# Performance work log

Measured on AMD Instinct MI355X. Metric: run time of the kernel, lower is better.

## Reference

```python
import jax, jax.numpy as jnp
import numpy as np

N, D_IN, D_OUT = 4096, 1024, 1024


def setup_inputs() -> dict:
    key = jax.random.key(0)
    kx, kq, kk, kv = jax.random.split(key, 4)
    s = 1.0 / np.sqrt(D_IN)
    return {
        "x": jax.random.normal(kx, (N, D_IN), dtype=jnp.float32),
        "Wq": jax.random.normal(kq, (D_OUT, D_IN), dtype=jnp.float32) * s,
        "Wk": jax.random.normal(kk, (D_OUT, D_IN), dtype=jnp.float32) * s,
        "Wv": jax.random.normal(kv, (D_OUT, D_IN), dtype=jnp.float32) * s,
    }


def reference(x, Wq, Wk, Wv):
    # nn.Linear(d_in, d_out, bias=False): y = x @ W.T with W: [d_out, d_in]
    q = x @ Wq.T            # [N, d_out]
    k = x @ Wk.T            # [N, d_out]
    v = x @ Wv.T            # [N, d_out]
    scores = q @ k.T        # [N, N]
    scale = 1.0 / jnp.sqrt(jnp.asarray(k.shape[-1], dtype=x.dtype))
    attn = jax.nn.softmax(scores * scale, axis=-1)
    return attn @ v         # [N, d_out]
```

## Files before the change

kernel.cpp:

```cpp
#include <hip/hip_runtime.h>


typedef __attribute__((ext_vector_type(8))) __bf16 bf16x8;
typedef __attribute__((ext_vector_type(4))) float floatx4;

#define GLB_AS __attribute__((address_space(1)))
#define LDS_AS __attribute__((address_space(3)))

static __device__ __forceinline__ unsigned short f2bf_u16(float f) {
  union { float f; unsigned u; } x; x.f = f;
  unsigned r = x.u;
  r += 0x7fffu + ((r >> 16) & 1u);
  return (unsigned short)(r >> 16);
}
static __device__ __forceinline__ float bf2f(unsigned short u) {
  union { unsigned u; float f; } x; x.u = ((unsigned)u) << 16; return x.f;
}

__global__ __launch_bounds__(256) void cast_all(const float* __restrict__ x,
                                                const float* __restrict__ Wq,
                                                const float* __restrict__ Wk,
                                                const float* __restrict__ Wv,
                                                unsigned short* __restrict__ xb,
                                                unsigned short* __restrict__ wb) {
  const int i = blockIdx.x * 256 + threadIdx.x;
  const int NX4 = 4096 * 1024 / 4;
  const int NW4 = 1024 * 1024 / 4;
  const float* src; unsigned short* dst; int k;
  if (i < NX4)                { src = x;  dst = xb;                   k = i; }
  else if (i < NX4 + NW4)     { src = Wq; dst = wb;                   k = i - NX4; }
  else if (i < NX4 + 2 * NW4) { src = Wk; dst = wb + 1024 * 1024;     k = i - NX4 - NW4; }
  else                        { src = Wv; dst = wb + 2 * 1024 * 1024; k = i - NX4 - 2 * NW4; }
  float4 v = reinterpret_cast<const float4*>(src)[k];
  ushort4 o = make_ushort4(f2bf_u16(v.x), f2bf_u16(v.y), f2bf_u16(v.z), f2bf_u16(v.w));
  reinterpret_cast<ushort4*>(dst)[k] = o;
}

struct GemmOuts { void* c[4]; int ldc[4]; };

template <int EPI>
__global__ __launch_bounds__(256, 2) void gemm_bt(const unsigned short* __restrict__ A,
                                                  const unsigned short* __restrict__ B,
                                                  GemmOuts outs, int lda, int ldb,
                                                  int klen, float scale) {
  __shared__ unsigned short sh[24576];
  const int t = threadIdx.x;
  const int w = t >> 6, lane = t & 63;
  const int wm = w >> 1, wn = w & 1;
  const int gx = gridDim.x;
  const int nwg = gx * gridDim.y;
  int bid = blockIdx.y * gx + blockIdx.x;
  bid = (bid & 7) * (nwg >> 3) + (bid >> 3);
  const int row0 = (bid / gx) * 256;
  const int col0 = (bid % gx) * 128;
  const int z = blockIdx.z;
  const int kstart = z * klen;
  const int NT = klen >> 5;

  const int srow = t >> 2;
  const int scbe = (((t & 3) ^ ((t >> 3) & 3)) << 3);
  const unsigned short* gA0 = A + (size_t)(row0 + srow) * lda + kstart + scbe;
  const unsigned short* gA1 = gA0 + (size_t)64 * lda;
  const unsigned short* gA2 = gA0 + (size_t)128 * lda;
  const unsigned short* gA3 = gA0 + (size_t)192 * lda;
  const unsigned short* gB0 = B + (size_t)(col0 + srow) * ldb + kstart + scbe;
  const unsigned short* gB1 = gB0 + (size_t)64 * ldb;

#define STAGE(tl_) do { \
    const int bb_ = ((tl_) & 1) * 12288; \
    __builtin_amdgcn_global_load_lds((const GLB_AS void*)(gA0 + (tl_) * 32), \
        (LDS_AS void*)&sh[bb_ + t * 8], 16, 0, 0); \
    __builtin_amdgcn_global_load_lds((const GLB_AS void*)(gA1 + (tl_) * 32), \
        (LDS_AS void*)&sh[bb_ + 2048 + t * 8], 16, 0, 0); \
    __builtin_amdgcn_global_load_lds((const GLB_AS void*)(gA2 + (tl_) * 32), \
        (LDS_AS void*)&sh[bb_ + 4096 + t * 8], 16, 0, 0); \
    __builtin_amdgcn_global_load_lds((const GLB_AS void*)(gA3 + (tl_) * 32), \
        (LDS_AS void*)&sh[bb_ + 6144 + t * 8], 16, 0, 0); \
    __builtin_amdgcn_global_load_lds((const GLB_AS void*)(gB0 + (tl_) * 32), \
        (LDS_AS void*)&sh[bb_ + 8192 + t * 8], 16, 0, 0); \
    __builtin_amdgcn_global_load_lds((const GLB_AS void*)(gB1 + (tl_) * 32), \
        (LDS_AS void*)&sh[bb_ + 10240 + t * 8], 16, 0, 0); \
  } while (0)

  const int fr = lane & 15;
  const int sg = (((lane >> 4) ^ ((lane >> 1) & 3)) << 3);
  int aofs[8], bofs[4];
#pragma unroll
  for (int mf = 0; mf < 8; ++mf) aofs[mf] = ((wm * 128 + mf * 16 + fr) << 5) + sg;
#pragma unroll
  for (int nf = 0; nf < 4; ++nf) bofs[nf] = 8192 + ((wn * 64 + nf * 16 + fr) << 5) + sg;

  floatx4 acc[8][4] = {};

  STAGE(0);

  for (int tile = 0; tile < NT; ++tile) {
    if (tile + 1 < NT) {
      STAGE(tile + 1);
      asm volatile("s_waitcnt vmcnt(6)" ::: "memory");
    } else {
      asm volatile("s_waitcnt vmcnt(0)" ::: "memory");
    }
    __builtin_amdgcn_s_barrier();

    const int bo = (tile & 1) * 12288;
    bf16x8 af[8], bf[4];
#pragma unroll
    for (int mf = 0; mf < 8; ++mf) af[mf] = *(const bf16x8*)&sh[bo + aofs[mf]];
#pragma unroll
    for (int nf = 0; nf < 4; ++nf) bf[nf] = *(const bf16x8*)&sh[bo + bofs[nf]];
#pragma unroll
    for (int mf = 0; mf < 8; ++mf)
#pragma unroll
      for (int nf = 0; nf < 4; ++nf)
        acc[mf][nf] = __builtin_amdgcn_mfma_f32_16x16x32_bf16(af[mf], bf[nf], acc[mf][nf], 0, 0, 0);

    __builtin_amdgcn_s_barrier();
  }
#undef STAGE

  const int er = (lane >> 4) * 4;
  const int ec = lane & 15;

  if (EPI == 0) {
    unsigned short* Cb = (unsigned short*)outs.c[z];
    const int ldc = outs.ldc[z];
#pragma unroll
    for (int mf = 0; mf < 8; ++mf)
#pragma unroll
      for (int nf = 0; nf < 4; ++nf)
#pragma unroll
        for (int r = 0; r < 4; ++r)
          Cb[(size_t)(row0 + wm * 128 + mf * 16 + er + r) * ldc +
             (col0 + wn * 64 + nf * 16 + ec)] = f2bf_u16(acc[mf][nf][r] * scale);
  } else if (EPI == 2) {
    unsigned short* Pb = (unsigned short*)outs.c[0];
    float* rsp = (float*)outs.c[1];
    const int ldc = outs.ldc[0];
    const int rj = ((col0 >> 7) * 2 + wn) * 4096;
#pragma unroll
    for (int mf = 0; mf < 8; ++mf) {
#pragma unroll
      for (int r = 0; r < 4; ++r) {
        const int m = row0 + wm * 128 + mf * 16 + er + r;
        float rsum = 0.f;
#pragma unroll
        for (int nf = 0; nf < 4; ++nf) {
          const float e = __expf(acc[mf][nf][r] * scale);
          Pb[(size_t)m * ldc + (col0 + wn * 64 + nf * 16 + ec)] = f2bf_u16(e);
          rsum += e;
        }
        rsum += __shfl_xor(rsum, 1);
        rsum += __shfl_xor(rsum, 2);
        rsum += __shfl_xor(rsum, 4);
        rsum += __shfl_xor(rsum, 8);
        if (ec == 0) rsp[rj + m] = rsum;
      }
    }
  } else {
    if (col0 < 2048) {
      unsigned short* qkb = (unsigned short*)outs.c[0];
#pragma unroll
      for (int mf = 0; mf < 8; ++mf)
#pragma unroll
        for (int nf = 0; nf < 4; ++nf)
#pragma unroll
          for (int r = 0; r < 4; ++r)
            qkb[(size_t)(row0 + wm * 128 + mf * 16 + er + r) * 2048 +
                (col0 + wn * 64 + nf * 16 + ec)] = f2bf_u16(acc[mf][nf][r] * scale);
    } else {
      unsigned short* vT = (unsigned short*)outs.c[1];
#pragma unroll
      for (int mf = 0; mf < 8; ++mf)
#pragma unroll
        for (int nf = 0; nf < 4; ++nf) {
          const int n = (col0 - 2048) + wn * 64 + nf * 16 + ec;
          const int mb = row0 + wm * 128 + mf * 16 + er;
          ushort4 o = make_ushort4(f2bf_u16(acc[mf][nf][0] * scale),
                                   f2bf_u16(acc[mf][nf][1] * scale),
                                   f2bf_u16(acc[mf][nf][2] * scale),
                                   f2bf_u16(acc[mf][nf][3] * scale));
          *reinterpret_cast<ushort4*>(&vT[(size_t)n * 4096 + mb]) = o;
        }
    }
  }
}

__global__ __launch_bounds__(256) void reduce_pv(float* __restrict__ out,
                                                 const unsigned short* __restrict__ p0,
                                                 const unsigned short* __restrict__ p1,
                                                 const float* __restrict__ rsp) {
  const int row = blockIdx.x;
  const int lane = threadIdx.x & 63;
  float s = rsp[lane * 4096 + row];
#pragma unroll
  for (int off = 32; off >= 1; off >>= 1) s += __shfl_xor(s, off);
  const float inv = 1.0f / s;
  const int idx = row * 256 + threadIdx.x;
  ushort4 a = ((const ushort4*)p0)[idx];
  ushort4 b = ((const ushort4*)p1)[idx];
  float4 o;
  o.x = (bf2f(a.x) + bf2f(b.x)) * inv;
  o.y = (bf2f(a.y) + bf2f(b.y)) * inv;
  o.z = (bf2f(a.z) + bf2f(b.z)) * inv;
  o.w = (bf2f(a.w) + bf2f(b.w)) * inv;
  ((float4*)out)[idx] = o;
}

extern "C" void kernel_launch(void* const* d_in, const int* in_sizes, int n_in,
                              void* d_out, int out_size, void* d_ws, size_t ws_size,
                              hipStream_t stream) {
  const float* x  = (const float*)d_in[0];
  const float* Wq = (const float*)d_in[1];
  const float* Wk = (const float*)d_in[2];
  const float* Wv = (const float*)d_in[3];
  float* out = (float*)d_out;

  const int N = 4096, D = 1024;

  char* ws = (char*)d_ws;
  unsigned short* P   = (unsigned short*)ws;
  unsigned short* qkb = (unsigned short*)(ws + (32u << 20));
  unsigned short* vT  = (unsigned short*)(ws + (48u << 20));
  unsigned short* xb  = (unsigned short*)(ws + (56u << 20));
  unsigned short* wb  = (unsigned short*)(ws + (64u << 20));
  float*          rsp = (float*)(ws + (70u << 20));
  unsigned short* p0  = xb;
  unsigned short* p1  = (unsigned short*)(ws + (72u << 20));

  cast_all<<<7168, 256, 0, stream>>>(x, Wq, Wk, Wv, xb, wb);

  GemmOuts oq; oq.c[0] = qkb; oq.c[1] = vT; oq.c[2] = oq.c[3] = qkb;
  oq.ldc[0] = 2048; oq.ldc[1] = 4096; oq.ldc[2] = oq.ldc[3] = 2048;
  gemm_bt<3><<<dim3(3 * D / 128, N / 256, 1), 256, 0, stream>>>(xb, wb, oq, D, D, D, 1.0f);

  GemmOuts os; os.c[0] = P; os.c[1] = rsp; os.c[2] = os.c[3] = P;
  os.ldc[0] = N; os.ldc[1] = 0; os.ldc[2] = os.ldc[3] = N;
  gemm_bt<2><<<dim3(N / 128, N / 256, 1), 256, 0, stream>>>(qkb, qkb + D, os, 2 * D, 2 * D, D, 0.03125f);

  GemmOuts op;
  op.c[0] = p0; op.ldc[0] = D;
  op.c[1] = p1; op.ldc[1] = D;
  op.c[2] = p0; op.ldc[2] = D;
  op.c[3] = p1; op.ldc[3] = D;
  gemm_bt<0><<<dim3(D / 128, N / 256, 2), 256, 0, stream>>>(P, vT, op, N, N, N / 2, 1.0f);

  reduce_pv<<<N, 256, 0, stream>>>(out, p0, p1, rsp);
}
```

Baseline: 142.8 us.

## Fuse split-K reduction and normalization into PV GEMM via atomic tile counters

Replaces the separate reduce_pv pass with a last-arriving-block scheme. Each split-K block of the PV GEMM writes its bf16 partial, bumps a per-tile atomic counter, and the second block to finish sums both partials and applies the softmax row normalization straight into the fp32 output. Row sums are pre-collapsed by a small kernel, and the counters are zeroed by an extra block in the cast kernel. This removes a full read/write pass and a launch, at the cost of fences, atomics, a tail imbalance on the finishing blocks, and a new small kernel.

```diff
diff --git a/kernel.cpp b/kernel.cpp
--- a/kernel.cpp
+++ b/kernel.cpp
@@ -22,10 +22,15 @@
                                                 const float* __restrict__ Wk,
                                                 const float* __restrict__ Wv,
                                                 unsigned short* __restrict__ xb,
-                                                unsigned short* __restrict__ wb) {
-  const int i = blockIdx.x * 256 + threadIdx.x;
+                                                unsigned short* __restrict__ wb,
+                                                int* __restrict__ cnt) {
   const int NX4 = 4096 * 1024 / 4;
   const int NW4 = 1024 * 1024 / 4;
+  if (blockIdx.x == 7168) {
+    if (threadIdx.x < 128) cnt[threadIdx.x] = 0;
+    return;
+  }
+  const int i = blockIdx.x * 256 + threadIdx.x;
   const float* src; unsigned short* dst; int k;
   if (i < NX4)                { src = x;  dst = xb;                   k = i; }
   else if (i < NX4 + NW4)     { src = Wq; dst = wb;                   k = i - NX4; }
@@ -36,7 +41,16 @@
   reinterpret_cast<ushort4*>(dst)[k] = o;
 }
 
-struct GemmOuts { void* c[4]; int ldc[4]; };
+__global__ __launch_bounds__(256) void collapse_rs(const float* __restrict__ rsp,
+                                                   float* __restrict__ rs) {
+  const int r = blockIdx.x * 256 + threadIdx.x;
+  float s = 0.f;
+#pragma unroll
+  for (int j = 0; j < 64; ++j) s += rsp[j * 4096 + r];
+  rs[r] = s;
+}
+
+struct GemmOuts { void* c[5]; int ldc0; };
 
 template <int EPI>
 __global__ __launch_bounds__(256, 2) void gemm_bt(const unsigned short* __restrict__ A,
@@ -44,6 +58,7 @@
                                                   GemmOuts outs, int lda, int ldb,
                                                   int klen, float scale) {
   __shared__ unsigned short sh[24576];
+  __shared__ int lf;
   const int t = threadIdx.x;
   const int w = t >> 6, lane = t & 63;
   const int wm = w >> 1, wn = w & 1;
@@ -123,20 +138,45 @@
   const int ec = lane & 15;
 
   if (EPI == 0) {
-    unsigned short* Cb = (unsigned short*)outs.c[z];
-    const int ldc = outs.ldc[z];
+    float* Of = (float*)outs.c[0];
+    unsigned short* myp = (unsigned short*)(z == 0 ? outs.c[1] : outs.c[2]);
+    const unsigned short* otp = (const unsigned short*)(z == 0 ? outs.c[2] : outs.c[1]);
+    const float* rsv = (const float*)outs.c[3];
+    int* cnt = (int*)outs.c[4];
+    const int tileid = (row0 >> 8) * gx + (col0 >> 7);
 #pragma unroll
     for (int mf = 0; mf < 8; ++mf)
 #pragma unroll
       for (int nf = 0; nf < 4; ++nf)
 #pragma unroll
         for (int r = 0; r < 4; ++r)
-          Cb[(size_t)(row0 + wm * 128 + mf * 16 + er + r) * ldc +
-             (col0 + wn * 64 + nf * 16 + ec)] = f2bf_u16(acc[mf][nf][r] * scale);
+          myp[(size_t)(row0 + wm * 128 + mf * 16 + er + r) * 1024 +
+              (col0 + wn * 64 + nf * 16 + ec)] = f2bf_u16(acc[mf][nf][r]);
+    __threadfence();
+    __syncthreads();
+    if (t == 0) lf = atomicAdd(cnt + tileid, 1);
+    __syncthreads();
+    if (lf == 1) {
+      __threadfence();
+#pragma unroll
+      for (int mf = 0; mf < 8; ++mf) {
+#pragma unroll
+        for (int r = 0; r < 4; ++r) {
+          const int m = row0 + wm * 128 + mf * 16 + er + r;
+          const float inv = 1.0f / rsv[m];
+#pragma unroll
+          for (int nf = 0; nf < 4; ++nf) {
+            const int n = col0 + wn * 64 + nf * 16 + ec;
+            const float own = bf2f(f2bf_u16(acc[mf][nf][r]));
+            Of[(size_t)m * 1024 + n] = (own + bf2f(otp[(size_t)m * 1024 + n])) * inv;
+          }
+        }
+      }
+    }
   } else if (EPI == 2) {
     unsigned short* Pb = (unsigned short*)outs.c[0];
     float* rsp = (float*)outs.c[1];
-    const int ldc = outs.ldc[0];
+    const int ldc = outs.ldc0;
     const int rj = ((col0 >> 7) * 2 + wn) * 4096;
 #pragma unroll
     for (int mf = 0; mf < 8; ++mf) {
@@ -167,7 +207,7 @@
 #pragma unroll
           for (int r = 0; r < 4; ++r)
             qkb[(size_t)(row0 + wm * 128 + mf * 16 + er + r) * 2048 +
-                (col0 + wn * 64 + nf * 16 + ec)] = f2bf_u16(acc[mf][nf][r] * scale);
+                (col0 + wn * 64 + nf * 16 + ec)] = f2bf_u16(acc[mf][nf][r]);
     } else {
       unsigned short* vT = (unsigned short*)outs.c[1];
 #pragma unroll
@@ -176,35 +216,12 @@
         for (int nf = 0; nf < 4; ++nf) {
           const int n = (col0 - 2048) + wn * 64 + nf * 16 + ec;
           const int mb = row0 + wm * 128 + mf * 16 + er;
-          ushort4 o = make_ushort4(f2bf_u16(acc[mf][nf][0] * scale),
-                                   f2bf_u16(acc[mf][nf][1] * scale),
-                                   f2bf_u16(acc[mf][nf][2] * scale),
-                                   f2bf_u16(acc[mf][nf][3] * scale));
+          ushort4 o = make_ushort4(f2bf_u16(acc[mf][nf][0]), f2bf_u16(acc[mf][nf][1]),
+                                   f2bf_u16(acc[mf][nf][2]), f2bf_u16(acc[mf][nf][3]));
           *reinterpret_cast<ushort4*>(&vT[(size_t)n * 4096 + mb]) = o;
         }
     }
   }
-}
-
-__global__ __launch_bounds__(256) void reduce_pv(float* __restrict__ out,
-                                                 const unsigned short* __restrict__ p0,
-                                                 const unsigned short* __restrict__ p1,
-                                                 const float* __restrict__ rsp) {
-  const int row = blockIdx.x;
-  const int lane = threadIdx.x & 63;
-  float s = rsp[lane * 4096 + row];
-#pragma unroll
-  for (int off = 32; off >= 1; off >>= 1) s += __shfl_xor(s, off);
-  const float inv = 1.0f / s;
-  const int idx = row * 256 + threadIdx.x;
-  ushort4 a = ((const ushort4*)p0)[idx];
-  ushort4 b = ((const ushort4*)p1)[idx];
-  float4 o;
-  o.x = (bf2f(a.x) + bf2f(b.x)) * inv;
-  o.y = (bf2f(a.y) + bf2f(b.y)) * inv;
-  o.z = (bf2f(a.z) + bf2f(b.z)) * inv;
-  o.w = (bf2f(a.w) + bf2f(b.w)) * inv;
-  ((float4*)out)[idx] = o;
 }
 
 extern "C" void kernel_launch(void* const* d_in, const int* in_sizes, int n_in,
@@ -225,25 +242,22 @@
   unsigned short* xb  = (unsigned short*)(ws + (56u << 20));
   unsigned short* wb  = (unsigned short*)(ws + (64u << 20));
   float*          rsp = (float*)(ws + (70u << 20));
+  float*          rs  = (float*)(ws + (71u << 20));
+  int*            cnt = (int*)(ws + (71u << 20) + 16384);
   unsigned short* p0  = xb;
   unsigned short* p1  = (unsigned short*)(ws + (72u << 20));
 
-  cast_all<<<7168, 256, 0, stream>>>(x, Wq, Wk, Wv, xb, wb);
-
-  GemmOuts oq; oq.c[0] = qkb; oq.c[1] = vT; oq.c[2] = oq.c[3] = qkb;
-  oq.ldc[0] = 2048; oq.ldc[1] = 4096; oq.ldc[2] = oq.ldc[3] = 2048;
+  cast_all<<<7169, 256, 0, stream>>>(x, Wq, Wk, Wv, xb, wb, cnt);
+
+  GemmOuts oq; oq.c[0] = qkb; oq.c[1] = vT; oq.c[2] = oq.c[3] = oq.c[4] = qkb; oq.ldc0 = 2048;
   gemm_bt<3><<<dim3(3 * D / 128, N / 256, 1), 256, 0, stream>>>(xb, wb, oq, D, D, D, 1.0f);
 
-  GemmOuts os; os.c[0] = P; os.c[1] = rsp; os.c[2] = os.c[3] = P;
-  os.ldc[0] = N; os.ldc[1] = 0; os.ldc[2] = os.ldc[3] = N;
+  GemmOuts os; os.c[0] = P; os.c[1] = rsp; os.c[2] = os.c[3] = os.c[4] = P; os.ldc0 = N;
   gemm_bt<2><<<dim3(N / 128, N / 256, 1), 256, 0, stream>>>(qkb, qkb + D, os, 2 * D, 2 * D, D, 0.03125f);
 
+  collapse_rs<<<16, 256, 0, stream>>>(rsp, rs);
+
   GemmOuts op;
-  op.c[0] = p0; op.ldc[0] = D;
-  op.c[1] = p1; op.ldc[1] = D;
-  op.c[2] = p0; op.ldc[2] = D;
-  op.c[3] = p1; op.ldc[3] = D;
+  op.c[0] = out; op.c[1] = p0; op.c[2] = p1; op.c[3] = rs; op.c[4] = cnt; op.ldc0 = D;
   gemm_bt<0><<<dim3(D / 128, N / 256, 2), 256, 0, stream>>>(P, vT, op, N, N, N / 2, 1.0f);
-
-  reduce_pv<<<N, 256, 0, stream>>>(out, p0, p1, rsp);
-}
+}
```

Result: slower. 221.3 us (+55.0%).
